# Kernel optimization log

Measured on AMD Instinct MI355X. Metric: run time of the kernel, lower is better.

## Reference

```python
import jax, jax.numpy as jnp
import numpy as np

D_EMBED = 1024


def setup_inputs() -> dict:
    key = jax.random.key(0)
    ks = jax.random.split(key, 8)
    B, S, D = 8, 2048, D_EMBED
    scale = 1.0 / np.sqrt(D)
    return {
        "embeddings": jax.random.normal(ks[0], (B, S, D), dtype=jnp.float32),
        "mask": jnp.zeros((B, S, S), dtype=jnp.float32),
        "Wq": jax.random.normal(ks[1], (D, D), dtype=jnp.float32) * scale,
        "bq": jax.random.normal(ks[2], (D,), dtype=jnp.float32) * 0.02,
        "Wk": jax.random.normal(ks[3], (D, D), dtype=jnp.float32) * scale,
        "bk": jax.random.normal(ks[4], (D,), dtype=jnp.float32) * 0.02,
        "Wv": jax.random.normal(ks[5], (D, D), dtype=jnp.float32) * scale,
        "bv": jax.random.normal(ks[6], (D,), dtype=jnp.float32) * 0.02,
    }


def reference(embeddings, mask, Wq, bq, Wk, bk, Wv, bv):
    # torch Linear: y = x @ W.T + b
    q = jnp.einsum('bsd,ed->bse', embeddings, Wq) + bq
    k = jnp.einsum('bsd,ed->bse', embeddings, Wk) + bk
    v = jnp.einsum('bsd,ed->bse', embeddings, Wv) + bv
    scores = jnp.einsum('bqd,bkd->bqk', q, k)
    # NOTE: faithful to source — mask added BEFORE scaling by 1/sqrt(d)
    scores = (scores + mask) * (1.0 / jnp.sqrt(jnp.float32(q.shape[-1])))
    attn = jax.nn.softmax(scores, axis=-1)
    return jnp.einsum('bqk,bkd->bqd', attn, v)
```

## Files before the change

kernel.cpp:

```cpp
#include <hip/hip_runtime.h>


#define B_SZ 8
#define SEQ  2048
#define DIM  1024
#define MROWS (B_SZ * SEQ)

typedef unsigned short u16;
typedef short short8 __attribute__((ext_vector_type(8)));
typedef unsigned short u16x4 __attribute__((ext_vector_type(4)));
typedef float f32x4 __attribute__((ext_vector_type(4)));

__device__ __forceinline__ u16 f2h(float x) {
  _Float16 h = (_Float16)x;
  union { _Float16 f; u16 u; } c; c.f = h; return c.u;
}
__device__ __forceinline__ float h2f(u16 u) {
  union { _Float16 f; u16 u; } c; c.u = u; return (float)c.f;
}

__device__ __forceinline__ int xcd_swz(int x, int nwg) {
  return (x & 7) * (nwg >> 3) + (x >> 3);
}

__device__ __forceinline__ void gload_lds16(const u16* g, u16* l) {
  __builtin_amdgcn_global_load_lds(
      (__attribute__((address_space(1))) void*)(g),
      (__attribute__((address_space(3))) void*)(l), 16, 0, 0);
}

__device__ __forceinline__ f32x4 mfma_f16(short8 a, short8 b, f32x4 c) {
  asm("v_mfma_f32_16x16x32_f16 %0, %1, %2, %0" : "+v"(c) : "v"(a), "v"(b));
  return c;
}

__device__ __forceinline__ void gemm256_core(const u16* __restrict__ Ag,
                                             const u16* __restrict__ Bg,
                                             int NT, size_t lda, size_t ldb,
                                             u16* sm, f32x4 (&acc)[8][4]) {
  const int tid = threadIdx.x;
  const int lane = tid & 63;
  const int wid = tid >> 6;
  const int wm8 = (wid >> 2) << 3;
  const int wn4 = (wid & 3) << 2;

  u16* sA = sm;
  u16* sB = sm + 32768;

  const int bb = (lane << 4) ^ (((lane >> 5) & 1) << 5);
  const int rins = bb >> 6;
  const int cins = (bb & 63) >> 1;
  const int s0 = wid, s1 = 8 + wid, s2 = 16 + wid, s3 = 24 + wid;
  const size_t aoff0 = (size_t)((s0 >> 1) * 16 + rins) * lda + ((s0 & 1) * 32 + cins);
  const size_t aoff1 = (size_t)((s1 >> 1) * 16 + rins) * lda + ((s1 & 1) * 32 + cins);
  const size_t aoff2 = (size_t)((s2 >> 1) * 16 + rins) * lda + ((s2 & 1) * 32 + cins);
  const size_t aoff3 = (size_t)((s3 >> 1) * 16 + rins) * lda + ((s3 & 1) * 32 + cins);
  const size_t boff0 = (size_t)((s0 >> 1) * 16 + rins) * ldb + ((s0 & 1) * 32 + cins);
  const size_t boff1 = (size_t)((s1 >> 1) * 16 + rins) * ldb + ((s1 & 1) * 32 + cins);
  const size_t boff2 = (size_t)((s2 >> 1) * 16 + rins) * ldb + ((s2 & 1) * 32 + cins);
  const size_t boff3 = (size_t)((s3 >> 1) * 16 + rins) * ldb + ((s3 & 1) * 32 + cins);
  const int wid512 = wid << 9;

  const int lof = ((lane & 15) << 6) + ((lane >> 4) << 4);
  const int loe = (lof ^ (((lane >> 3) & 1) << 5)) >> 1;

#define ISSUE_A(j, nb, kt) \
  gload_lds16(Ag + aoff##j + (size_t)(kt) * 64, sA + (nb) * 16384 + (j) * 4096 + wid512)
#define ISSUE_B(j, nb, kt) \
  gload_lds16(Bg + boff##j + (size_t)(kt) * 64, sB + (nb) * 16384 + (j) * 4096 + wid512)

  ISSUE_B(0, 0, 0); ISSUE_B(1, 0, 0); ISSUE_B(2, 0, 0); ISSUE_B(3, 0, 0);
  ISSUE_A(0, 0, 0); ISSUE_A(2, 0, 0); ISSUE_A(1, 0, 0); ISSUE_A(3, 0, 0);

  int buf = 0;
  for (int kt = 0; kt < NT; ++kt) {
    const int nk = kt + 1;
    const bool pre = nk < NT;
    const int nb = buf ^ 1;
    asm volatile("s_waitcnt vmcnt(2)" ::: "memory");
    __builtin_amdgcn_s_barrier();
    asm volatile("" ::: "memory");
    const u16* bufA = sA + buf * 16384;
    const u16* bufB = sB + buf * 16384;
    short8 bf[4][2];
#pragma unroll
    for (int n = 0; n < 4; ++n) {
      bf[n][0] = *(const short8*)(bufB + (wn4 + n) * 1024 + loe);
      bf[n][1] = *(const short8*)(bufB + (wn4 + n) * 1024 + 512 + loe);
    }
    {
      short8 af[2][2];
#pragma unroll
      for (int m = 0; m < 2; ++m) {
        af[m][0] = *(const short8*)(bufA + (wm8 + m) * 1024 + loe);
        af[m][1] = *(const short8*)(bufA + (wm8 + m) * 1024 + 512 + loe);
      }
      if (pre) {
        ISSUE_B(0, nb, nk); ISSUE_B(1, nb, nk); ISSUE_B(2, nb, nk); ISSUE_B(3, nb, nk);
        ISSUE_A(0, nb, nk); ISSUE_A(2, nb, nk); ISSUE_A(1, nb, nk); ISSUE_A(3, nb, nk);
      }
      __builtin_amdgcn_s_setprio(1);
#pragma unroll
      for (int m = 0; m < 2; ++m)
#pragma unroll
        for (int n = 0; n < 4; ++n) {
          acc[m][n] = mfma_f16(af[m][0], bf[n][0], acc[m][n]);
          acc[m][n] = mfma_f16(af[m][1], bf[n][1], acc[m][n]);
        }
      __builtin_amdgcn_s_setprio(0);
    }
    {
      short8 af[2][2];
#pragma unroll
      for (int m = 0; m < 2; ++m) {
        af[m][0] = *(const short8*)(bufA + (wm8 + 2 + m) * 1024 + loe);
        af[m][1] = *(const short8*)(bufA + (wm8 + 2 + m) * 1024 + 512 + loe);
      }
      __builtin_amdgcn_s_setprio(1);
#pragma unroll
      for (int m = 0; m < 2; ++m)
#pragma unroll
        for (int n = 0; n < 4; ++n) {
          acc[2 + m][n] = mfma_f16(af[m][0], bf[n][0], acc[2 + m][n]);
          acc[2 + m][n] = mfma_f16(af[m][1], bf[n][1], acc[2 + m][n]);
        }
      __builtin_amdgcn_s_setprio(0);
    }
    if (pre) {
      asm volatile("s_waitcnt vmcnt(8)" ::: "memory");
    } else {
      asm volatile("s_waitcnt vmcnt(0)" ::: "memory");
    }
    __builtin_amdgcn_s_barrier();
    asm volatile("" ::: "memory");
    {
      short8 af[2][2];
#pragma unroll
      for (int m = 0; m < 2; ++m) {
        af[m][0] = *(const short8*)(bufA + (wm8 + 4 + m) * 1024 + loe);
        af[m][1] = *(const short8*)(bufA + (wm8 + 4 + m) * 1024 + 512 + loe);
      }
      __builtin_amdgcn_s_setprio(1);
#pragma unroll
      for (int m = 0; m < 2; ++m)
#pragma unroll
        for (int n = 0; n < 4; ++n) {
          acc[4 + m][n] = mfma_f16(af[m][0], bf[n][0], acc[4 + m][n]);
          acc[4 + m][n] = mfma_f16(af[m][1], bf[n][1], acc[4 + m][n]);
        }
      __builtin_amdgcn_s_setprio(0);
    }
    {
      short8 af[2][2];
#pragma unroll
      for (int m = 0; m < 2; ++m) {
        af[m][0] = *(const short8*)(bufA + (wm8 + 6 + m) * 1024 + loe);
        af[m][1] = *(const short8*)(bufA + (wm8 + 6 + m) * 1024 + 512 + loe);
      }
      __builtin_amdgcn_s_setprio(1);
#pragma unroll
      for (int m = 0; m < 2; ++m)
#pragma unroll
        for (int n = 0; n < 4; ++n) {
          acc[6 + m][n] = mfma_f16(af[m][0], bf[n][0], acc[6 + m][n]);
          acc[6 + m][n] = mfma_f16(af[m][1], bf[n][1], acc[6 + m][n]);
        }
      __builtin_amdgcn_s_setprio(0);
    }
    buf ^= 1;
  }
  asm volatile("s_nop 7\n\ts_nop 7\n\ts_nop 7" ::);
#undef ISSUE_A
#undef ISSUE_B
}

__device__ __forceinline__ void gemm128_core(const u16* A, const u16* Bt, int K,
                                             int lda, int ldb, f32x4 (&acc)[4][4],
                                             u16* sA, u16* sB) {
  const int tid = threadIdx.x;
  const int lane = tid & 63;
  const int wid = tid >> 6;
  const int wr = wid >> 1;
  const int wc = wid & 1;
  const int srow = tid >> 2;
  const int scol = (tid & 3) << 3;
  const u16* ga0 = A + (size_t)srow * lda + scol;
  const u16* ga1 = A + (size_t)(srow + 64) * lda + scol;
  const u16* gb0 = Bt + (size_t)srow * ldb + scol;
  const u16* gb1 = Bt + (size_t)(srow + 64) * ldb + scol;
  u16* la0 = sA + (wid << 9);
  u16* la1 = sA + 2048 + (wid << 9);
  u16* lb0 = sB + (wid << 9);
  u16* lb1 = sB + 2048 + (wid << 9);
  const u16* pa = sA + (size_t)((wr << 6) + (lane & 15)) * 32 + ((lane >> 4) << 3);
  const u16* pb = sB + (size_t)((wc << 6) + (lane & 15)) * 32 + ((lane >> 4) << 3);
  const int ksteps = K >> 5;
  for (int kt = 0; kt < ksteps; ++kt) {
    gload_lds16(ga0, la0);
    gload_lds16(ga1, la1);
    gload_lds16(gb0, lb0);
    gload_lds16(gb1, lb1);
    ga0 += 32; ga1 += 32; gb0 += 32; gb1 += 32;
    __syncthreads();
    short8 a[4], b[4];
#pragma unroll
    for (int i = 0; i < 4; ++i) a[i] = *(const short8*)(pa + (i << 9));
#pragma unroll
    for (int i = 0; i < 4; ++i) b[i] = *(const short8*)(pb + (i << 9));
#pragma unroll
    for (int mi = 0; mi < 4; ++mi)
#pragma unroll
      for (int ni = 0; ni < 4; ++ni)
        acc[mi][ni] = mfma_f16(a[mi], b[ni], acc[mi][ni]);
    __syncthreads();
  }
  asm volatile("s_nop 7\n\ts_nop 7\n\ts_nop 7" ::);
}

__global__ __launch_bounds__(256) void prep_kernel(const float* __restrict__ emb,
                                                   const float* __restrict__ Wq,
                                                   const float* __restrict__ Wk,
                                                   const float* __restrict__ Wv,
                                                   const float* __restrict__ bq,
                                                   u16* __restrict__ emb16,
                                                   u16* __restrict__ WqT,
                                                   u16* __restrict__ WkT,
                                                   u16* __restrict__ Wv16,
                                                   float* __restrict__ w) {
  __shared__ float t[64][65];
  const int b = blockIdx.x;
  const int tid = threadIdx.x;
  if (b < 16384) {
    int i = b * 256 + tid;
    float4 v = ((const float4*)emb)[i];
    u16x4 o;
    o[0] = f2h(v.x); o[1] = f2h(v.y); o[2] = f2h(v.z); o[3] = f2h(v.w);
    ((u16x4*)emb16)[i] = o;
  } else if (b < 16896) {
    const int b2 = b - 16384;
    const float* src = (b2 >> 8) ? Wk : Wq;
    u16* dst = (b2 >> 8) ? WkT : WqT;
    const int rem = b2 & 255;
    const int r0 = (rem >> 4) * 64;
    const int c0 = (rem & 15) * 64;
    const int tr = tid >> 4;
    const int c4 = (tid & 15) << 2;
#pragma unroll
    for (int i = 0; i < 4; ++i) {
      float4 x = *(const float4*)(src + (size_t)(r0 + tr + 16 * i) * 1024 + c0 + c4);
      t[tr + 16 * i][c4 + 0] = x.x;
      t[tr + 16 * i][c4 + 1] = x.y;
      t[tr + 16 * i][c4 + 2] = x.z;
      t[tr + 16 * i][c4 + 3] = x.w;
    }
    __syncthreads();
#pragma unroll
    for (int i = 0; i < 4; ++i) {
      int dr = tr + 16 * i;
      u16x4 y;
      y[0] = f2h(t[c4 + 0][dr]);
      y[1] = f2h(t[c4 + 1][dr]);
      y[2] = f2h(t[c4 + 2][dr]);
      y[3] = f2h(t[c4 + 3][dr]);
      *(u16x4*)(dst + (size_t)(c0 + dr) * 1024 + r0 + c4) = y;
    }
  } else if (b < 17920) {
    int i = (b - 16896) * 256 + tid;
    float4 v = ((const float4*)Wv)[i];
    u16x4 o;
    o[0] = f2h(v.x); o[1] = f2h(v.y); o[2] = f2h(v.z); o[3] = f2h(v.w);
    ((u16x4*)Wv16)[i] = o;
  } else {
    const int e = (b - 17920) * 256 + tid;
    float s = 0.f;
    for (int c = 0; c < 1024; c += 4) {
      s += Wk[(size_t)c * 1024 + e] * bq[c];
      s += Wk[(size_t)(c + 1) * 1024 + e] * bq[c + 1];
      s += Wk[(size_t)(c + 2) * 1024 + e] * bq[c + 2];
      s += Wk[(size_t)(c + 3) * 1024 + e] * bq[c + 3];
    }
    w[e] = s * 0.03125f;
  }
}

__global__ __launch_bounds__(256) void cmt_kernel(const u16* __restrict__ emb16,
                                                  const u16* __restrict__ WqT,
                                                  const u16* __restrict__ WkT,
                                                  const float* __restrict__ w,
                                                  float* __restrict__ c,
                                                  float* __restrict__ MtP) {
  __shared__ __align__(16) u16 smem[8192];
  const int b = blockIdx.x;
  const int tid = threadIdx.x;
  if (b < 4096) {
    float* sw = (float*)smem;
    for (int i = tid; i < 1024; i += 256) sw[i] = w[i];
    __syncthreads();
    const int wv = tid >> 6, lane = tid & 63;
    const int r = b * 4 + wv;
    const u16* row = emb16 + (size_t)r * 1024;
    float s = 0.f;
#pragma unroll
    for (int it = 0; it < 2; ++it) {
      int d = lane * 8 + it * 512;
      short8 v = *(const short8*)(row + d);
#pragma unroll
      for (int j = 0; j < 8; ++j) s += h2f((u16)v[j]) * sw[d + j];
    }
#pragma unroll
    for (int off = 1; off < 64; off <<= 1) s += __shfl_xor(s, off);
    if (lane == 0) c[r] = s;
  } else {
    const int b2 = b - 4096;
    const int tile = b2 >> 2;
    const int kc = b2 & 3;
    const int m0 = (tile >> 3) * 128;
    const int n0 = (tile & 7) * 128;
    f32x4 acc[4][4] = {};
    gemm128_core(WkT + (size_t)m0 * 1024 + kc * 256,
                 WqT + (size_t)n0 * 1024 + kc * 256, 256, 1024, 1024,
                 acc, smem, smem + 4096);
    const int lane = tid & 63, wid = tid >> 6;
    const int wr = wid >> 1, wc = wid & 1;
    float* plane = MtP + (size_t)kc * 1024 * 1024;
#pragma unroll
    for (int mi = 0; mi < 4; ++mi)
#pragma unroll
      for (int ni = 0; ni < 4; ++ni)
#pragma unroll
        for (int j = 0; j < 4; ++j) {
          int row = m0 + (wr << 6) + mi * 16 + ((lane >> 4) << 2) + j;
          int col = n0 + (wc << 6) + ni * 16 + (lane & 15);
          plane[(size_t)row * 1024 + col] = acc[mi][ni][j];
        }
  }
}

__global__ __launch_bounds__(256) void mtred_kernel(const float* __restrict__ MtP,
                                                    u16* __restrict__ Mt) {
  const size_t i = (size_t)blockIdx.x * 1024 + threadIdx.x * 4;
  float4 a = *(const float4*)(MtP + i);
  float4 b = *(const float4*)(MtP + 1048576 + i);
  float4 cc = *(const float4*)(MtP + 2097152 + i);
  float4 d = *(const float4*)(MtP + 3145728 + i);
  u16x4 o;
  o[0] = f2h((a.x + b.x + cc.x + d.x) * 0.03125f);
  o[1] = f2h((a.y + b.y + cc.y + d.y) * 0.03125f);
  o[2] = f2h((a.z + b.z + cc.z + d.z) * 0.03125f);
  o[3] = f2h((a.w + b.w + cc.w + d.w) * 0.03125f);
  *(u16x4*)(Mt + i) = o;
}

__global__ __launch_bounds__(512) void proj256_kernel(const u16* __restrict__ emb16,
                                                      const u16* __restrict__ Mt,
                                                      const u16* __restrict__ Wv16,
                                                      const float* __restrict__ bv,
                                                      u16* __restrict__ G,
                                                      u16* __restrict__ vT) {
  __shared__ __align__(16) u16 sm[65536];
  const int wg = xcd_swz(blockIdx.x, 512);
  const int lane = threadIdx.x & 63, wid = threadIdx.x >> 6;
  f32x4 acc[8][4] = {};
  if (wg < 256) {
    const int m0 = (wg >> 2) * 256;
    const int n0 = (wg & 3) * 256;
    gemm256_core(emb16 + (size_t)m0 * 1024, Mt + (size_t)n0 * 1024, 16, 1024, 1024,
                 sm, acc);
    const int rb = m0 + ((wid >> 2) << 7) + ((lane >> 4) << 2);
    const int cb = n0 + ((wid & 3) << 6) + (lane & 15);
#pragma unroll
    for (int m = 0; m < 8; ++m)
#pragma unroll
      for (int n = 0; n < 4; ++n)
#pragma unroll
        for (int j = 0; j < 4; ++j)
          G[(size_t)(rb + m * 16 + j) * 1024 + (cb + n * 16)] = f2h(acc[m][n][j]);
  } else {
    const int r = wg - 256;
    const int m0 = (r & 3) * 256;
    const int n0 = (r >> 2) * 256;
    gemm256_core(Wv16 + (size_t)m0 * 1024, emb16 + (size_t)n0 * 1024, 16, 1024, 1024,
                 sm, acc);
    const int rb = m0 + ((wid >> 2) << 7) + ((lane >> 4) << 2);
    const int cb = n0 + ((wid & 3) << 6) + (lane & 15);
#pragma unroll
    for (int m = 0; m < 8; ++m)
#pragma unroll
      for (int n = 0; n < 4; ++n)
#pragma unroll
        for (int j = 0; j < 4; ++j) {
          int d = rb + m * 16 + j;
          int kg = cb + n * 16;
          int bi = kg >> 11, s = kg & 2047;
          vT[((size_t)bi << 21) + ((size_t)d << 11) + s] = f2h(acc[m][n][j] + bv[d]);
        }
  }
}

__global__ __launch_bounds__(512) void scores256_kernel(const u16* __restrict__ G,
                                                        const u16* __restrict__ emb16,
                                                        const float* __restrict__ c,
                                                        u16* __restrict__ scH) {
  __shared__ __align__(16) u16 sm[65536];
  const int wg = xcd_swz(blockIdx.x, 512);
  const int b = wg >> 6;
  const int m0 = ((wg >> 3) & 7) * 256;
  const int n0 = (wg & 7) * 256;
  f32x4 acc[8][4] = {};
  gemm256_core(G + ((size_t)b * SEQ + m0) * DIM, emb16 + ((size_t)b * SEQ + n0) * DIM,
               16, DIM, DIM, sm, acc);
  const int lane = threadIdx.x & 63, wid = threadIdx.x >> 6;
  const int rb = m0 + ((wid >> 2) << 7) + ((lane >> 4) << 2);
  const int cb = n0 + ((wid & 3) << 6) + (lane & 15);
  float cn[4];
#pragma unroll
  for (int n = 0; n < 4; ++n) cn[n] = c[(size_t)b * SEQ + cb + n * 16];
#pragma unroll
  for (int m = 0; m < 8; ++m)
#pragma unroll
    for (int n = 0; n < 4; ++n)
#pragma unroll
      for (int j = 0; j < 4; ++j) {
        size_t idx = ((size_t)b * SEQ + rb + m * 16 + j) * SEQ + (cb + n * 16);
        scH[idx] = f2h(acc[m][n][j] + cn[n]);
      }
}

__global__ __launch_bounds__(256) void softmax_kernel(u16* __restrict__ scH,
                                                      const float* __restrict__ mask) {
  __shared__ float red[8];
  const size_t row = blockIdx.x;
  u16* rowp = scH + row * SEQ;
  const float* mrow = mask + row * SEQ;
  const int tid = threadIdx.x;
  short8 raw = *(const short8*)(rowp + tid * 8);
  float4 m0 = ((const float4*)mrow)[2 * tid];
  float4 m1 = ((const float4*)mrow)[2 * tid + 1];
  float mk[8] = {m0.x, m0.y, m0.z, m0.w, m1.x, m1.y, m1.z, m1.w};
  float f[8];
#pragma unroll
  for (int j = 0; j < 8; ++j) f[j] = h2f((u16)raw[j]) + mk[j] * 0.03125f;
  float mx = f[0];
#pragma unroll
  for (int j = 1; j < 8; ++j) mx = fmaxf(mx, f[j]);
#pragma unroll
  for (int off = 1; off < 64; off <<= 1) mx = fmaxf(mx, __shfl_xor(mx, off));
  const int wid = tid >> 6, lane = tid & 63;
  if (lane == 0) red[wid] = mx;
  __syncthreads();
  mx = fmaxf(fmaxf(red[0], red[1]), fmaxf(red[2], red[3]));
  float e[8];
  float s = 0.f;
#pragma unroll
  for (int j = 0; j < 8; ++j) {
    e[j] = __expf(f[j] - mx);
    s += e[j];
  }
#pragma unroll
  for (int off = 1; off < 64; off <<= 1) s += __shfl_xor(s, off);
  if (lane == 0) red[4 + wid] = s;
  __syncthreads();
  s = (red[4] + red[5]) + (red[6] + red[7]);
  const float inv = 1.f / s;
  short8 o;
#pragma unroll
  for (int j = 0; j < 8; ++j) o[j] = (short)f2h(e[j] * inv);
  *(short8*)(rowp + tid * 8) = o;
}

__global__ __launch_bounds__(512) void pv256_kernel(const u16* __restrict__ pr,
                                                    const u16* __restrict__ vt,
                                                    float* __restrict__ out) {
  __shared__ __align__(16) u16 sm[65536];
  const int wg = xcd_swz(blockIdx.x, 256);
  const int b = wg >> 5;
  const int m0 = ((wg >> 2) & 7) * 256;
  const int n0 = (wg & 3) * 256;
  f32x4 acc[8][4] = {};
  gemm256_core(pr + ((size_t)b * SEQ + m0) * SEQ, vt + ((size_t)b * DIM + n0) * SEQ,
               32, SEQ, SEQ, sm, acc);
  const int lane = threadIdx.x & 63, wid = threadIdx.x >> 6;
  const int rb = m0 + ((wid >> 2) << 7) + ((lane >> 4) << 2);
  const int cb = n0 + ((wid & 3) << 6) + (lane & 15);
#pragma unroll
  for (int m = 0; m < 8; ++m)
#pragma unroll
    for (int n = 0; n < 4; ++n)
#pragma unroll
      for (int j = 0; j < 4; ++j)
        out[((size_t)b * SEQ + rb + m * 16 + j) * DIM + (cb + n * 16)] = acc[m][n][j];
}

extern "C" void kernel_launch(void* const* d_in, const int* in_sizes, int n_in,
                              void* d_out, int out_size, void* d_ws, size_t ws_size,
                              hipStream_t stream) {
  const float* emb  = (const float*)d_in[0];
  const float* mask = (const float*)d_in[1];
  const float* Wq   = (const float*)d_in[2];
  const float* bq   = (const float*)d_in[3];
  const float* Wk   = (const float*)d_in[4];
  const float* bk   = (const float*)d_in[5];
  const float* Wv   = (const float*)d_in[6];
  const float* bv   = (const float*)d_in[7];
  float* out = (float*)d_out;
  (void)bk;

  const size_t M1 = 1024 * 1024;
  u16* scH   = (u16*)d_ws;
  u16* emb16 = scH + 32 * M1;
  u16* WqT   = emb16 + 16 * M1;
  u16* WkT   = WqT + M1;
  u16* Wv16  = WkT + M1;
  u16* Mt    = Wv16 + M1;
  u16* G     = Mt + M1;
  u16* vT    = G + 16 * M1;
  float* MtP = (float*)(vT + 16 * M1);
  float* w   = MtP + 4 * M1;
  float* c   = w + 1024;

  prep_kernel<<<17924, 256, 0, stream>>>(emb, Wq, Wk, Wv, bq, emb16, WqT, WkT, Wv16, w);
  cmt_kernel<<<4352, 256, 0, stream>>>(emb16, WqT, WkT, w, c, MtP);
  mtred_kernel<<<1024, 256, 0, stream>>>(MtP, Mt);

  proj256_kernel<<<512, 512, 0, stream>>>(emb16, Mt, Wv16, bv, G, vT);

  scores256_kernel<<<512, 512, 0, stream>>>(G, emb16, c, scH);
  softmax_kernel<<<MROWS, 256, 0, stream>>>(scH, mask);
  pv256_kernel<<<256, 512, 0, stream>>>((const u16*)scH, vT, out);
}
```

Measured before the change: 328.8 us.

## Split GEMM prefetch issues across sub-phases and parallelize bias-weight reduction with atomics

The GEMM main loop now issues the next tile's global-to-LDS loads in four pairs interleaved with the four MFMA sub-blocks, adding extra barriers and a tighter vmcnt wait. This spreads memory traffic across compute instead of bursting all loads at the start. Separately, the Wk·bq reduction in prep_kernel is split over 64 blocks that each handle 16 rows with float4 loads and atomicAdd, replacing 4 blocks that each looped over 1024 rows. The bias-vector buffer is cleared with a memset first. The trade-off is extra barriers, an added memset launch, and atomics whose float summation order is nondeterministic.

```diff
diff --git a/kernel.cpp b/kernel.cpp
--- a/kernel.cpp
+++ b/kernel.cpp
@@ -83,22 +83,19 @@
     const u16* bufA = sA + buf * 16384;
     const u16* bufB = sB + buf * 16384;
     short8 bf[4][2];
-#pragma unroll
-    for (int n = 0; n < 4; ++n) {
-      bf[n][0] = *(const short8*)(bufB + (wn4 + n) * 1024 + loe);
-      bf[n][1] = *(const short8*)(bufB + (wn4 + n) * 1024 + 512 + loe);
-    }
     {
+#pragma unroll
+      for (int n = 0; n < 4; ++n) {
+        bf[n][0] = *(const short8*)(bufB + (wn4 + n) * 1024 + loe);
+        bf[n][1] = *(const short8*)(bufB + (wn4 + n) * 1024 + 512 + loe);
+      }
       short8 af[2][2];
 #pragma unroll
       for (int m = 0; m < 2; ++m) {
         af[m][0] = *(const short8*)(bufA + (wm8 + m) * 1024 + loe);
         af[m][1] = *(const short8*)(bufA + (wm8 + m) * 1024 + 512 + loe);
       }
-      if (pre) {
-        ISSUE_B(0, nb, nk); ISSUE_B(1, nb, nk); ISSUE_B(2, nb, nk); ISSUE_B(3, nb, nk);
-        ISSUE_A(0, nb, nk); ISSUE_A(2, nb, nk); ISSUE_A(1, nb, nk); ISSUE_A(3, nb, nk);
-      }
+      if (pre) { ISSUE_B(0, nb, nk); ISSUE_B(1, nb, nk); }
       __builtin_amdgcn_s_setprio(1);
 #pragma unroll
       for (int m = 0; m < 2; ++m)
@@ -109,6 +106,8 @@
         }
       __builtin_amdgcn_s_setprio(0);
     }
+    __builtin_amdgcn_s_barrier();
+    asm volatile("" ::: "memory");
     {
       short8 af[2][2];
 #pragma unroll
@@ -116,6 +115,7 @@
         af[m][0] = *(const short8*)(bufA + (wm8 + 2 + m) * 1024 + loe);
         af[m][1] = *(const short8*)(bufA + (wm8 + 2 + m) * 1024 + 512 + loe);
       }
+      if (pre) { ISSUE_B(2, nb, nk); ISSUE_B(3, nb, nk); }
       __builtin_amdgcn_s_setprio(1);
 #pragma unroll
       for (int m = 0; m < 2; ++m)
@@ -127,7 +127,7 @@
       __builtin_amdgcn_s_setprio(0);
     }
     if (pre) {
-      asm volatile("s_waitcnt vmcnt(8)" ::: "memory");
+      asm volatile("s_waitcnt vmcnt(4)" ::: "memory");
     } else {
       asm volatile("s_waitcnt vmcnt(0)" ::: "memory");
     }
@@ -140,6 +140,7 @@
         af[m][0] = *(const short8*)(bufA + (wm8 + 4 + m) * 1024 + loe);
         af[m][1] = *(const short8*)(bufA + (wm8 + 4 + m) * 1024 + 512 + loe);
       }
+      if (pre) { ISSUE_A(0, nb, nk); ISSUE_A(2, nb, nk); }
       __builtin_amdgcn_s_setprio(1);
 #pragma unroll
       for (int m = 0; m < 2; ++m)
@@ -150,6 +151,8 @@
         }
       __builtin_amdgcn_s_setprio(0);
     }
+    __builtin_amdgcn_s_barrier();
+    asm volatile("" ::: "memory");
     {
       short8 af[2][2];
 #pragma unroll
@@ -157,6 +160,7 @@
         af[m][0] = *(const short8*)(bufA + (wm8 + 6 + m) * 1024 + loe);
         af[m][1] = *(const short8*)(bufA + (wm8 + 6 + m) * 1024 + 512 + loe);
       }
+      if (pre) { ISSUE_A(1, nb, nk); ISSUE_A(3, nb, nk); }
       __builtin_amdgcn_s_setprio(1);
 #pragma unroll
       for (int m = 0; m < 2; ++m)
@@ -271,15 +275,20 @@
     o[0] = f2h(v.x); o[1] = f2h(v.y); o[2] = f2h(v.z); o[3] = f2h(v.w);
     ((u16x4*)Wv16)[i] = o;
   } else {
-    const int e = (b - 17920) * 256 + tid;
-    float s = 0.f;
-    for (int c = 0; c < 1024; c += 4) {
-      s += Wk[(size_t)c * 1024 + e] * bq[c];
-      s += Wk[(size_t)(c + 1) * 1024 + e] * bq[c + 1];
-      s += Wk[(size_t)(c + 2) * 1024 + e] * bq[c + 2];
-      s += Wk[(size_t)(c + 3) * 1024 + e] * bq[c + 3];
-    }
-    w[e] = s * 0.03125f;
+    const int rb = b - 17920;
+    const int e0 = tid << 2;
+    float a0 = 0.f, a1 = 0.f, a2 = 0.f, a3 = 0.f;
+#pragma unroll
+    for (int r = 0; r < 16; ++r) {
+      int row = rb * 16 + r;
+      float4 x = *(const float4*)(Wk + (size_t)row * 1024 + e0);
+      float s = bq[row];
+      a0 += x.x * s; a1 += x.y * s; a2 += x.z * s; a3 += x.w * s;
+    }
+    atomicAdd(&w[e0 + 0], a0 * 0.03125f);
+    atomicAdd(&w[e0 + 1], a1 * 0.03125f);
+    atomicAdd(&w[e0 + 2], a2 * 0.03125f);
+    atomicAdd(&w[e0 + 3], a3 * 0.03125f);
   }
 }
 
@@ -518,7 +527,8 @@
   float* w   = MtP + 4 * M1;
   float* c   = w + 1024;
 
-  prep_kernel<<<17924, 256, 0, stream>>>(emb, Wq, Wk, Wv, bq, emb16, WqT, WkT, Wv16, w);
+  hipMemsetAsync(w, 0, 1024 * sizeof(float), stream);
+  prep_kernel<<<17984, 256, 0, stream>>>(emb, Wq, Wk, Wv, bq, emb16, WqT, WkT, Wv16, w);
   cmt_kernel<<<4352, 256, 0, stream>>>(emb16, WqT, WkT, w, c, MtP);
   mtred_kernel<<<1024, 256, 0, stream>>>(MtP, Mt);
 
```

Result: faster. 298.6 us (-9.2%).
